# Kernel optimization log

Hardware: AMD Instinct MI355X
Metric: run time of the kernel (lower is better)

Reference implementation:

```python
import jax, jax.numpy as jnp
import numpy as np

B, T, E, V = 128, 24, 512, 30000
H2 = 2 * 512  # LSTMCell hidden size = 2*hidden_size per original code
IN = 2 * E    # token embedding concat image feature


def setup_inputs() -> dict:
    key = jax.random.key(0)
    ks = jax.random.split(key, 9)
    s = lambda fan: 1.0 / np.sqrt(fan)
    return {
        "features": jax.random.normal(ks[0], (B, E), jnp.float32),
        "captions": jax.random.randint(ks[1], (B, T), 0, V),
        "pad_idx": 0,
        "emb": jax.random.normal(ks[2], (V, E), jnp.float32),
        "W_ih": jax.random.uniform(ks[3], (4 * H2, IN), jnp.float32, -s(H2), s(H2)),
        "W_hh": jax.random.uniform(ks[4], (4 * H2, H2), jnp.float32, -s(H2), s(H2)),
        "b_ih": jax.random.uniform(ks[5], (4 * H2,), jnp.float32, -s(H2), s(H2)),
        "b_hh": jax.random.uniform(ks[6], (4 * H2,), jnp.float32, -s(H2), s(H2)),
        "W_out": jax.random.uniform(ks[7], (V, H2), jnp.float32, -s(H2), s(H2)),
        "b_out": jax.random.uniform(ks[8], (V,), jnp.float32, -s(H2), s(H2)),
    }


def reference(features, captions, pad_idx, emb, W_ih, W_hh, b_ih, b_hh, W_out, b_out):
    b = captions.shape[0]
    tok = emb[captions]                                   # [B,T,E]
    pad = jnp.broadcast_to(emb[pad_idx][None, None, :], (b, 1, E))
    seq = jnp.concatenate([pad, tok], axis=1)             # [B,T+1,E]
    feat = jnp.broadcast_to(features[:, None, :], (b, seq.shape[1], features.shape[1]))
    x = jnp.concatenate([seq, feat], axis=2)              # [B,T+1,2E]

    # precompute input-side gate projections for all timesteps (batched GEMM)
    xg = jnp.einsum('bti,gi->btg', x, W_ih) + b_ih + b_hh  # [B,T+1,4*H2]

    def step(carry, xg_t):
        h, c = carry
        g = xg_t + h @ W_hh.T                             # [B,4*H2]
        i, f, gg, o = jnp.split(g, 4, axis=-1)            # torch gate order i,f,g,o
        i, f, o = jax.nn.sigmoid(i), jax.nn.sigmoid(f), jax.nn.sigmoid(o)
        c = f * c + i * jnp.tanh(gg)
        h = o * jnp.tanh(c)
        return (h, c), h

    h0 = jnp.zeros((b, H2), x.dtype)
    c0 = jnp.zeros((b, H2), x.dtype)
    _, hs = jax.lax.scan(step, (h0, c0), jnp.swapaxes(xg, 0, 1))  # [T+1,B,H2]
    hs = jnp.swapaxes(hs, 0, 1)                           # [B,T+1,H2]

    logits = jnp.einsum('bth,vh->btv', hs, W_out) + b_out  # [B,T+1,V]
    predicted = jnp.transpose(logits[:, :-1, :], (0, 2, 1))  # [B,V,T]
    return predicted
```

## Files before the change

### kernel.cpp

```cpp
#include <hip/hip_runtime.h>
#include <hip/hip_bf16.h>
#include <math.h>

typedef unsigned short ushort_t;
typedef unsigned long long u64;
typedef __bf16 bf16x8 __attribute__((ext_vector_type(8)));
typedef float f32x4 __attribute__((ext_vector_type(4)));

#define BB 128
#define TT 24
#define EE 512
#define VV 30000
#define HH 1024
#define GG 4096
#define MM (BB*TT)
#define MPAD 30208

static __device__ __forceinline__ ushort_t f2bf(float x) {
  __hip_bfloat16 h = __float2bfloat16(x);
  return __builtin_bit_cast(ushort_t, h);
}

static __device__ __forceinline__ void gld_lds16(const void* g, void* l) {
  __builtin_amdgcn_global_load_lds((const __attribute__((address_space(1))) void*)g,
                                   (__attribute__((address_space(3))) void*)l, 16, 0, 0);
}


__global__ void cast_bf16_k(const float* __restrict__ s, ushort_t* __restrict__ d, int n4) {
  int i = blockIdx.x * blockDim.x + threadIdx.x;
  int stride = gridDim.x * blockDim.x;
  for (; i < n4; i += stride) {
    float4 v = reinterpret_cast<const float4*>(s)[i];
    ushort4 o;
    o.x = f2bf(v.x); o.y = f2bf(v.y); o.z = f2bf(v.z); o.w = f2bf(v.w);
    reinterpret_cast<ushort4*>(d)[i] = o;
  }
}

__global__ void bias_sum_k(const float* __restrict__ bi, const float* __restrict__ bh,
                           float* __restrict__ bs) {
  int i = blockIdx.x * blockDim.x + threadIdx.x;
  if (i < GG) bs[i] = bi[i] + bh[i];
}

__global__ void build_xa_k(const float* __restrict__ emb, const int* __restrict__ captions,
                           const int* __restrict__ pad_idx, const float* __restrict__ features,
                           ushort_t* __restrict__ xa) {
  int row = blockIdx.x;
  int t = row >> 7;
  int b = row & 127;
  int cap = (t == 0) ? pad_idx[0] : captions[b * TT + (t - 1)];
  const float* s0 = emb + (size_t)cap * EE;
  const float* s1 = features + (size_t)b * EE;
  ushort_t* d = xa + (size_t)row * (2 * EE);
  for (int e = threadIdx.x; e < EE; e += 256) {
    d[e] = f2bf(s0[e]);
    d[EE + e] = f2bf(s1[e]);
  }
}

__global__ void zero_bar_k(int* __restrict__ bar) {
  for (int i = threadIdx.x; i < 768; i += 256)
    __hip_atomic_store(&bar[i], 0, __ATOMIC_RELAXED, __HIP_MEMORY_SCOPE_AGENT);
}

__global__ __launch_bounds__(256) void gemm_xg(
    const ushort_t* __restrict__ A,
    const ushort_t* __restrict__ Bm,
    const float* __restrict__ bias,
    float* __restrict__ out,
    int M, int N, int swn, int xn_cnt)
{
  constexpr int K = 1024;
  __shared__ __align__(16) ushort_t As[2][8192];
  __shared__ __align__(16) ushort_t Bs[2][8192];
  const int bid = blockIdx.x;
  const int xcd = bid & 7, c = bid >> 3;
  const int xn = xcd % xn_cnt, xm = xcd / xn_cnt;
  const int nblk = xn * swn + (c % swn);
  const int n0 = nblk * 128;
  const int m0 = (xm * ((gridDim.x >> 3) / swn) + (c / swn)) * 128;
  const int tid = threadIdx.x, wid = tid >> 6, lane = tid & 63;
  const int wm = (wid >> 1) * 64, wn_ = (wid & 1) * 64;
  const int srow = lane >> 3;
  const int scolsw = ((lane & 7) ^ srow) * 8;
  const int rr = lane & 15, l4 = lane >> 4;
  const int swz = (rr & 7) << 4;
  const int col0 = (((l4 << 4) ^ swz) >> 1);
  const int col1 = (((64 | (l4 << 4)) ^ swz) >> 1);

  f32x4 acc[4][4] = {};

  auto stage = [&](int buf, int k0) {
    #pragma unroll
    for (int p = 0; p < 4; ++p) {
      int ch = p * 4 + wid;
      int row = ch * 8 + srow;
      gld_lds16(A + (size_t)(m0 + row) * K + k0 + scolsw, &As[buf][ch * 512]);
      gld_lds16(Bm + (size_t)(n0 + row) * K + k0 + scolsw, &Bs[buf][ch * 512]);
    }
  };

  stage(0, 0);
  int cur = 0;
  for (int tau = 0; tau < 16; ++tau) {
    if (tau < 15) {
      stage(cur ^ 1, (tau + 1) * 64);
      asm volatile("s_waitcnt vmcnt(8)" ::: "memory");
    } else {
      asm volatile("s_waitcnt vmcnt(0)" ::: "memory");
    }
    __builtin_amdgcn_s_barrier();
    const ushort_t* Ac = As[cur];
    const ushort_t* Bc = Bs[cur];
    #pragma unroll
    for (int kk = 0; kk < 2; ++kk) {
      const int ce = kk ? col1 : col0;
      bf16x8 af[4], bfv[4];
      #pragma unroll
      for (int i = 0; i < 4; ++i)
        af[i] = *reinterpret_cast<const bf16x8*>(Ac + (wm + i * 16 + rr) * 64 + ce);
      #pragma unroll
      for (int j = 0; j < 4; ++j)
        bfv[j] = *reinterpret_cast<const bf16x8*>(Bc + (wn_ + j * 16 + rr) * 64 + ce);
      #pragma unroll
      for (int i = 0; i < 4; ++i)
        #pragma unroll
        for (int j = 0; j < 4; ++j)
          acc[i][j] = __builtin_amdgcn_mfma_f32_16x16x32_bf16(af[i], bfv[j], acc[i][j], 0, 0, 0);
    }
    asm volatile("" ::: "memory");
    __builtin_amdgcn_s_barrier();
    cur ^= 1;
  }

  const int l16 = lane & 15;
  const int t_blk = m0 >> 7;
  #pragma unroll
  for (int i = 0; i < 4; ++i) {
    #pragma unroll
    for (int j = 0; j < 4; ++j) {
      int n = n0 + wn_ + j * 16 + l16;
      float bv = bias[n];
      #pragma unroll
      for (int r = 0; r < 4; ++r) {
        int b = wm + i * 16 + l4 * 4 + r;
        out[((size_t)t_blk * GG + n) * BB + b] = acc[i][j][r] + bv;
      }
    }
  }
}

__global__ __launch_bounds__(512) void gemm256_logits(
    const ushort_t* __restrict__ A,
    const ushort_t* __restrict__ Bm,
    const float* __restrict__ bias,
    float* __restrict__ out)
{
  constexpr int K = 1024, NT = 16;
  __shared__ __align__(16) ushort_t As[2][16384];
  __shared__ __align__(16) ushort_t Bs[2][16384];
  const int bid = blockIdx.x;
  const int g = (bid & 7) * 177 + (bid >> 3);
  const int m0 = (g / 12) * 256, n0 = (g % 12) * 256;
  const int tid = threadIdx.x, wid = tid >> 6, lane = tid & 63;
  const int wm2 = wid >> 2, wn4 = wid & 3;
  const int rr = lane & 15, l4 = lane >> 4;

  f32x4 acc[8][4] = {};

  auto stage = [&](int buf, int kt, int ct) {
    const int k0 = kt * 64;
    #pragma unroll
    for (int l = 0; l < 2; ++l) {
      int f = l * 512 + tid;
      int lr = f >> 3;
      int ecol = k0 + (((f & 7) ^ (lr & 7)) * 8);
      if (ct == 0 || ct == 3) {
        int cc = (ct == 3);
        int grow = (lr & 63) + ((lr >> 6) << 7) + cc * 64;
        gld_lds16(A + (size_t)(m0 + grow) * K + ecol,
                  &As[buf][cc * 8192 + (l * 512 + wid * 64) * 8]);
      } else {
        int cc = ct - 1;
        int grow = ((lr >> 5) << 6) + cc * 32 + (lr & 31);
        gld_lds16(Bm + (size_t)(n0 + grow) * K + ecol,
                  &Bs[buf][cc * 8192 + (l * 512 + wid * 64) * 8]);
      }
    }
  };
  auto rdA = [&](int buf, int mf, int kk) -> bf16x8 {
    int rl = wm2 * 64 + (mf & 3) * 16 + rr;
    return *reinterpret_cast<const bf16x8*>(
        &As[buf][(mf >> 2) * 8192 + rl * 64 + (((kk * 4 + l4) ^ (rr & 7)) * 8)]);
  };
  auto rdB = [&](int buf, int nf, int kk) -> bf16x8 {
    int rl = wn4 * 32 + (nf & 1) * 16 + rr;
    return *reinterpret_cast<const bf16x8*>(
        &Bs[buf][(nf >> 1) * 8192 + rl * 64 + (((kk * 4 + l4) ^ (rr & 7)) * 8)]);
  };

  #pragma unroll
  for (int hh = 0; hh < 4; ++hh) stage(0, 0, hh);
  asm volatile("s_waitcnt vmcnt(4)" ::: "memory");
  __builtin_amdgcn_s_barrier();

  bf16x8 aF[4][2], bF[2][2], bF2[2][2];
  int cur = 0;
  for (int g2 = 0; g2 < NT; ++g2) {
    const int buf = cur, bufn = cur ^ 1;
    const int ktn = (g2 + 1 < NT) ? g2 + 1 : g2;
    #pragma unroll
    for (int mf = 0; mf < 4; ++mf) { aF[mf][0] = rdA(buf, mf, 0); aF[mf][1] = rdA(buf, mf, 1); }
    #pragma unroll
    for (int nf = 0; nf < 2; ++nf) { bF[nf][0] = rdB(buf, nf, 0); bF[nf][1] = rdB(buf, nf, 1); }
    stage(bufn, ktn, 0);
    __builtin_amdgcn_s_barrier();
    asm volatile("s_waitcnt lgkmcnt(0)" ::: "memory");
    __builtin_amdgcn_sched_barrier(0);
    __builtin_amdgcn_s_setprio(1);
    #pragma unroll
    for (int mf = 0; mf < 4; ++mf)
      #pragma unroll
      for (int nf = 0; nf < 2; ++nf) {
        acc[mf][nf] = __builtin_amdgcn_mfma_f32_16x16x32_bf16(aF[mf][0], bF[nf][0], acc[mf][nf], 0, 0, 0);
        acc[mf][nf] = __builtin_amdgcn_mfma_f32_16x16x32_bf16(aF[mf][1], bF[nf][1], acc[mf][nf], 0, 0, 0);
      }
    __builtin_amdgcn_s_setprio(0);
    asm volatile("s_waitcnt vmcnt(4)" ::: "memory");
    __builtin_amdgcn_s_barrier();
    #pragma unroll
    for (int nf = 0; nf < 2; ++nf) { bF2[nf][0] = rdB(buf, 2 + nf, 0); bF2[nf][1] = rdB(buf, 2 + nf, 1); }
    stage(bufn, ktn, 1);
    __builtin_amdgcn_s_barrier();
    asm volatile("s_waitcnt lgkmcnt(0)" ::: "memory");
    __builtin_amdgcn_sched_barrier(0);
    __builtin_amdgcn_s_setprio(1);
    #pragma unroll
    for (int mf = 0; mf < 4; ++mf)
      #pragma unroll
      for (int nf = 0; nf < 2; ++nf) {
        acc[mf][2 + nf] = __builtin_amdgcn_mfma_f32_16x16x32_bf16(aF[mf][0], bF2[nf][0], acc[mf][2 + nf], 0, 0, 0);
        acc[mf][2 + nf] = __builtin_amdgcn_mfma_f32_16x16x32_bf16(aF[mf][1], bF2[nf][1], acc[mf][2 + nf], 0, 0, 0);
      }
    __builtin_amdgcn_s_setprio(0);
    asm volatile("s_waitcnt vmcnt(4)" ::: "memory");
    __builtin_amdgcn_s_barrier();
    #pragma unroll
    for (int mf = 0; mf < 4; ++mf) { aF[mf][0] = rdA(buf, 4 + mf, 0); aF[mf][1] = rdA(buf, 4 + mf, 1); }
    stage(bufn, ktn, 2);
    __builtin_amdgcn_s_barrier();
    asm volatile("s_waitcnt lgkmcnt(0)" ::: "memory");
    __builtin_amdgcn_sched_barrier(0);
    __builtin_amdgcn_s_setprio(1);
    #pragma unroll
    for (int mf = 0; mf < 4; ++mf)
      #pragma unroll
      for (int nf = 0; nf < 2; ++nf) {
        acc[4 + mf][nf] = __builtin_amdgcn_mfma_f32_16x16x32_bf16(aF[mf][0], bF[nf][0], acc[4 + mf][nf], 0, 0, 0);
        acc[4 + mf][nf] = __builtin_amdgcn_mfma_f32_16x16x32_bf16(aF[mf][1], bF[nf][1], acc[4 + mf][nf], 0, 0, 0);
      }
    __builtin_amdgcn_s_setprio(0);
    __builtin_amdgcn_s_barrier();
    stage(bufn, ktn, 3);
    __builtin_amdgcn_s_barrier();
    __builtin_amdgcn_s_setprio(1);
    #pragma unroll
    for (int mf = 0; mf < 4; ++mf)
      #pragma unroll
      for (int nf = 0; nf < 2; ++nf) {
        acc[4 + mf][2 + nf] = __builtin_amdgcn_mfma_f32_16x16x32_bf16(aF[mf][0], bF2[nf][0], acc[4 + mf][2 + nf], 0, 0, 0);
        acc[4 + mf][2 + nf] = __builtin_amdgcn_mfma_f32_16x16x32_bf16(aF[mf][1], bF2[nf][1], acc[4 + mf][2 + nf], 0, 0, 0);
      }
    __builtin_amdgcn_s_setprio(0);
    asm volatile("s_waitcnt vmcnt(4)" ::: "memory");
    __builtin_amdgcn_s_barrier();
    cur ^= 1;
  }
  asm volatile("s_waitcnt vmcnt(0)" ::: "memory");

  const int vbase = m0 + wm2 * 128;
  const int nbase = n0 + wn4 * 64;
  #pragma unroll
  for (int mf = 0; mf < 8; ++mf) {
    #pragma unroll
    for (int r = 0; r < 4; ++r) {
      int v = vbase + mf * 16 + l4 * 4 + r;
      if (v < VV) {
        float bv = bias[v];
        #pragma unroll
        for (int nf = 0; nf < 4; ++nf) {
          int n = nbase + nf * 16 + rr;
          int bb = n / TT, tq = n - bb * TT;
          out[(size_t)bb * ((size_t)VV * TT) + (size_t)v * TT + tq] = acc[mf][nf][r] + bv;
        }
      }
    }
  }
}

__global__ __launch_bounds__(512, 1) void lstm_seq_k(
    const ushort_t* __restrict__ Whh,
    const float* __restrict__ xgT,
    ushort_t* __restrict__ hs,
    int* __restrict__ bar)
{
  __shared__ f32x4 red[6][64][4];
  const int tid = threadIdx.x, wid = tid >> 6, lane = tid & 63;
  const int l16 = lane & 15, l4 = lane >> 4;
  const int bid = blockIdx.x;
  const int jblk = bid & 63, mblk = bid >> 6;
  const int j0 = jblk * 16, m0 = mblk * 32;
  const int ks = wid >> 1;
  const int msub = (wid & 1) * 16;
  int* flags = bar;
  int* rel = bar + 256;

  bf16x8 Breg[4][8];
  #pragma unroll
  for (int g = 0; g < 4; ++g) {
    const ushort_t* bp = Whh + ((size_t)(g * 1024 + j0 + l16) << 10) + ks * 256 + l4 * 8;
    #pragma unroll
    for (int kc = 0; kc < 8; ++kc)
      Breg[g][kc] = *reinterpret_cast<const bf16x8*>(bp + kc * 32);
  }
  const int arow = m0 + msub + l16;
  float c_reg[4] = {0.f, 0.f, 0.f, 0.f};

  for (int t = 0; t < TT; ++t) {
    f32x4 acc[4] = {};
    f32x4 xv[4];
    if (ks == 0) {
      const float* xp = xgT + ((size_t)(t * GG + j0 + l16)) * BB + m0 + msub + l4 * 4;
      #pragma unroll
      for (int g = 0; g < 4; ++g)
        xv[g] = *reinterpret_cast<const f32x4*>(xp + (size_t)g * 1024 * BB);
    }
    if (t > 0) {
      const u64* Ab = reinterpret_cast<const u64*>(
          hs + (((size_t)arow * TT + (t - 1)) << 10) + ks * 256 + l4 * 8);
      bf16x8 afs[8];
      #pragma unroll
      for (int kc = 0; kc < 8; ++kc) {
        union { u64 q[2]; bf16x8 v; } u;
        u.q[0] = __hip_atomic_load(Ab + kc * 8,     __ATOMIC_RELAXED, __HIP_MEMORY_SCOPE_AGENT);
        u.q[1] = __hip_atomic_load(Ab + kc * 8 + 1, __ATOMIC_RELAXED, __HIP_MEMORY_SCOPE_AGENT);
        afs[kc] = u.v;
      }
      #pragma unroll
      for (int kc = 0; kc < 8; ++kc)
        #pragma unroll
        for (int g = 0; g < 4; ++g)
          acc[g] = __builtin_amdgcn_mfma_f32_16x16x32_bf16(afs[kc], Breg[g][kc], acc[g], 0, 0, 0);
    }
    if (ks != 0) {
      int slot = (ks - 1) * 2 + (wid & 1);
      #pragma unroll
      for (int g = 0; g < 4; ++g) red[slot][lane][g] = acc[g];
    }
    __syncthreads();
    if (ks == 0) {
      #pragma unroll
      for (int s = 0; s < 3; ++s)
        #pragma unroll
        for (int g = 0; g < 4; ++g)
          acc[g] += red[s * 2 + (wid & 1)][lane][g];
      #pragma unroll
      for (int r = 0; r < 4; ++r) {
        int b = m0 + msub + l4 * 4 + r;
        float gi = acc[0][r] + xv[0][r];
        float gf = acc[1][r] + xv[1][r];
        float gg = acc[2][r] + xv[2][r];
        float go = acc[3][r] + xv[3][r];
        gi = 1.f / (1.f + expf(-gi));
        gf = 1.f / (1.f + expf(-gf));
        go = 1.f / (1.f + expf(-go));
        float cn = gf * c_reg[r] + gi * tanhf(gg);
        c_reg[r] = cn;
        float hn = go * tanhf(cn);
        unsigned hv = (unsigned)f2bf(hn);
        unsigned pv = (unsigned)__shfl_xor((int)hv, 1);
        if (!(l16 & 1)) {
          unsigned pk = (hv & 0xffffu) | (pv << 16);
          __hip_atomic_store(
              reinterpret_cast<unsigned*>(hs + (((size_t)b * TT + t) << 10) + j0 + l16),
              pk, __ATOMIC_RELAXED, __HIP_MEMORY_SCOPE_AGENT);
        }
      }
    }
    if (t < TT - 1) {
      __syncthreads();
      if (bid == 0) {
        if (wid == 0) {
          if (lane == 0)
            __hip_atomic_store(&flags[0], t + 1, __ATOMIC_RELAXED, __HIP_MEMORY_SCOPE_AGENT);
          for (;;) {
            int a0 = __hip_atomic_load(&flags[lane],       __ATOMIC_RELAXED, __HIP_MEMORY_SCOPE_AGENT);
            int a1 = __hip_atomic_load(&flags[lane +  64], __ATOMIC_RELAXED, __HIP_MEMORY_SCOPE_AGENT);
            int a2 = __hip_atomic_load(&flags[lane + 128], __ATOMIC_RELAXED, __HIP_MEMORY_SCOPE_AGENT);
            int a3 = __hip_atomic_load(&flags[lane + 192], __ATOMIC_RELAXED, __HIP_MEMORY_SCOPE_AGENT);
            int mn = min(min(a0, a1), min(a2, a3));
            if (__all(mn >= t + 1)) break;
            __builtin_amdgcn_s_sleep(2);
          }
          if (lane < 8)
            __hip_atomic_store(&rel[lane * 64], t + 1, __ATOMIC_RELAXED, __HIP_MEMORY_SCOPE_AGENT);
        }
      } else {
        if (tid == 0) {
          __hip_atomic_store(&flags[bid], t + 1, __ATOMIC_RELAXED, __HIP_MEMORY_SCOPE_AGENT);
          while (__hip_atomic_load(&rel[(bid & 7) * 64], __ATOMIC_RELAXED, __HIP_MEMORY_SCOPE_AGENT) < t + 1)
            __builtin_amdgcn_s_sleep(4);
        }
      }
      __syncthreads();
    }
  }
}


extern "C" void kernel_launch(void* const* d_in, const int* in_sizes, int n_in,
                              void* d_out, int out_size, void* d_ws, size_t ws_size,
                              hipStream_t stream) {
  const float* features = (const float*)d_in[0];
  const int*   captions = (const int*)d_in[1];
  const int*   pad_idx  = (const int*)d_in[2];
  const float* emb      = (const float*)d_in[3];
  const float* W_ih     = (const float*)d_in[4];
  const float* W_hh     = (const float*)d_in[5];
  const float* b_ih     = (const float*)d_in[6];
  const float* b_hh     = (const float*)d_in[7];
  const float* W_out    = (const float*)d_in[8];
  const float* b_out    = (const float*)d_in[9];
  float* out = (float*)d_out;

  char* w = (char*)d_ws;
  auto carve = [&](size_t bytes) {
    char* p = w;
    w += (bytes + 255) & ~(size_t)255;
    return p;
  };
  ushort_t* Wih_b  = (ushort_t*)carve((size_t)GG * HH * 2);
  ushort_t* Whh_b  = (ushort_t*)carve((size_t)GG * HH * 2);
  ushort_t* Wout_b = (ushort_t*)carve((size_t)MPAD * HH * 2);
  ushort_t* xa     = (ushort_t*)carve((size_t)MM * HH * 2);
  float*    xgT    = (float*)carve((size_t)MM * GG * 4);
  ushort_t* hs     = (ushort_t*)carve((size_t)MM * HH * 2);
  float*    bsum   = (float*)carve((size_t)GG * 4);
  int*      bar    = (int*)carve(4096);

  cast_bf16_k<<<dim3(1024), 256, 0, stream>>>(W_ih, Wih_b, GG * HH / 4);
  cast_bf16_k<<<dim3(1024), 256, 0, stream>>>(W_hh, Whh_b, GG * HH / 4);
  cast_bf16_k<<<dim3(2048), 256, 0, stream>>>(W_out, Wout_b, VV * HH / 4);
  bias_sum_k<<<dim3(16), 256, 0, stream>>>(b_ih, b_hh, bsum);
  build_xa_k<<<dim3(MM), 256, 0, stream>>>(emb, captions, pad_idx, features, xa);
  zero_bar_k<<<dim3(1), 256, 0, stream>>>(bar);

  gemm_xg<<<dim3(768), 256, 0, stream>>>(xa, Wih_b, bsum, xgT, MM, GG, 8, 4);

  lstm_seq_k<<<dim3(256), 512, 0, stream>>>(Whh_b, xgT, hs, bar);

  gemm256_logits<<<dim3(1416), 512, 0, stream>>>(Wout_b, hs, b_out, out);
}
```

Before: 563.3 us.

## Fuse prep casts, swap xg GEMM operands, use flat barrier in LSTM

Merges the three weight-cast kernels and the bias-sum kernel into one launch. It swaps the operands of the input-gate GEMM so the gate dimension indexes rows, with a new block-to-tile mapping and a matching output layout. The LSTM's centralized barrier (block 0 gathers and releases) is replaced by a flat barrier where each block polls only the 64 flags for its own m-block, which is meant to cut per-step sync latency. The logits epilogue hoists the division used in output index computation out of the store loop.

```diff
diff --git a/kernel.cpp b/kernel.cpp
--- a/kernel.cpp
+++ b/kernel.cpp
@@ -26,22 +26,29 @@
                                    (__attribute__((address_space(3))) void*)l, 16, 0, 0);
 }
 
-
-__global__ void cast_bf16_k(const float* __restrict__ s, ushort_t* __restrict__ d, int n4) {
-  int i = blockIdx.x * blockDim.x + threadIdx.x;
-  int stride = gridDim.x * blockDim.x;
-  for (; i < n4; i += stride) {
+__global__ void prep_k(const float* __restrict__ Wih, const float* __restrict__ Whh,
+                       const float* __restrict__ Wout,
+                       const float* __restrict__ bi, const float* __restrict__ bh,
+                       ushort_t* __restrict__ Wih_b, ushort_t* __restrict__ Whh_b,
+                       ushort_t* __restrict__ Wout_b, float* __restrict__ bs) {
+  const int bid = blockIdx.x, tid = threadIdx.x;
+  const float* s; ushort_t* d; int n4, i0, stride;
+  if (bid < 2048) {
+    s = Wout; d = Wout_b; n4 = VV * HH / 4; i0 = bid * 256 + tid; stride = 2048 * 256;
+  } else if (bid < 2560) {
+    s = Wih; d = Wih_b; n4 = GG * HH / 4; i0 = (bid - 2048) * 256 + tid; stride = 512 * 256;
+  } else if (bid < 3072) {
+    s = Whh; d = Whh_b; n4 = GG * HH / 4; i0 = (bid - 2560) * 256 + tid; stride = 512 * 256;
+  } else {
+    for (int i = tid; i < GG; i += 256) bs[i] = bi[i] + bh[i];
+    return;
+  }
+  for (int i = i0; i < n4; i += stride) {
     float4 v = reinterpret_cast<const float4*>(s)[i];
     ushort4 o;
     o.x = f2bf(v.x); o.y = f2bf(v.y); o.z = f2bf(v.z); o.w = f2bf(v.w);
     reinterpret_cast<ushort4*>(d)[i] = o;
   }
-}
-
-__global__ void bias_sum_k(const float* __restrict__ bi, const float* __restrict__ bh,
-                           float* __restrict__ bs) {
-  int i = blockIdx.x * blockDim.x + threadIdx.x;
-  if (i < GG) bs[i] = bi[i] + bh[i];
 }
 
 __global__ void build_xa_k(const float* __restrict__ emb, const int* __restrict__ captions,
@@ -61,7 +68,7 @@
 }
 
 __global__ void zero_bar_k(int* __restrict__ bar) {
-  for (int i = threadIdx.x; i < 768; i += 256)
+  for (int i = threadIdx.x; i < 1024; i += 256)
     __hip_atomic_store(&bar[i], 0, __ATOMIC_RELAXED, __HIP_MEMORY_SCOPE_AGENT);
 }
 
@@ -69,18 +76,15 @@
     const ushort_t* __restrict__ A,
     const ushort_t* __restrict__ Bm,
     const float* __restrict__ bias,
-    float* __restrict__ out,
-    int M, int N, int swn, int xn_cnt)
+    float* __restrict__ out)
 {
   constexpr int K = 1024;
   __shared__ __align__(16) ushort_t As[2][8192];
   __shared__ __align__(16) ushort_t Bs[2][8192];
   const int bid = blockIdx.x;
-  const int xcd = bid & 7, c = bid >> 3;
-  const int xn = xcd % xn_cnt, xm = xcd / xn_cnt;
-  const int nblk = xn * swn + (c % swn);
-  const int n0 = nblk * 128;
-  const int m0 = (xm * ((gridDim.x >> 3) / swn) + (c / swn)) * 128;
+  const int g = (bid & 7) * 96 + (bid >> 3);
+  const int m0 = (g / 24) * 128;
+  const int n0 = (g % 24) * 128;
   const int tid = threadIdx.x, wid = tid >> 6, lane = tid & 63;
   const int wm = (wid >> 1) * 64, wn_ = (wid & 1) * 64;
   const int srow = lane >> 3;
@@ -136,17 +140,16 @@
   }
 
   const int l16 = lane & 15;
-  const int t_blk = m0 >> 7;
   #pragma unroll
   for (int i = 0; i < 4; ++i) {
     #pragma unroll
-    for (int j = 0; j < 4; ++j) {
-      int n = n0 + wn_ + j * 16 + l16;
-      float bv = bias[n];
-      #pragma unroll
-      for (int r = 0; r < 4; ++r) {
-        int b = wm + i * 16 + l4 * 4 + r;
-        out[((size_t)t_blk * GG + n) * BB + b] = acc[i][j][r] + bv;
+    for (int r = 0; r < 4; ++r) {
+      int gi = m0 + wm + i * 16 + l4 * 4 + r;
+      float bv = bias[gi];
+      #pragma unroll
+      for (int j = 0; j < 4; ++j) {
+        int col = n0 + wn_ + j * 16 + l16;
+        out[((size_t)(col >> 7) * GG + gi) * BB + (col & 127)] = acc[i][j][r] + bv;
       }
     }
   }
@@ -282,6 +285,13 @@
 
   const int vbase = m0 + wm2 * 128;
   const int nbase = n0 + wn4 * 64;
+  size_t obase[4];
+  #pragma unroll
+  for (int nf = 0; nf < 4; ++nf) {
+    int n = nbase + nf * 16 + rr;
+    int bb = n / TT, tq = n - bb * TT;
+    obase[nf] = (size_t)bb * ((size_t)VV * TT) + tq;
+  }
   #pragma unroll
   for (int mf = 0; mf < 8; ++mf) {
     #pragma unroll
@@ -290,11 +300,8 @@
       if (v < VV) {
         float bv = bias[v];
         #pragma unroll
-        for (int nf = 0; nf < 4; ++nf) {
-          int n = nbase + nf * 16 + rr;
-          int bb = n / TT, tq = n - bb * TT;
-          out[(size_t)bb * ((size_t)VV * TT) + (size_t)v * TT + tq] = acc[mf][nf][r] + bv;
-        }
+        for (int nf = 0; nf < 4; ++nf)
+          out[obase[nf] + (size_t)v * TT] = acc[mf][nf][r] + bv;
       }
     }
   }
@@ -315,7 +322,7 @@
   const int ks = wid >> 1;
   const int msub = (wid & 1) * 16;
   int* flags = bar;
-  int* rel = bar + 256;
+  const int fidx = (mblk << 6) | (ks << 4) | l16;
 
   bf16x8 Breg[4][8];
   #pragma unroll
@@ -391,30 +398,13 @@
     }
     if (t < TT - 1) {
       __syncthreads();
-      if (bid == 0) {
-        if (wid == 0) {
-          if (lane == 0)
-            __hip_atomic_store(&flags[0], t + 1, __ATOMIC_RELAXED, __HIP_MEMORY_SCOPE_AGENT);
-          for (;;) {
-            int a0 = __hip_atomic_load(&flags[lane],       __ATOMIC_RELAXED, __HIP_MEMORY_SCOPE_AGENT);
-            int a1 = __hip_atomic_load(&flags[lane +  64], __ATOMIC_RELAXED, __HIP_MEMORY_SCOPE_AGENT);
-            int a2 = __hip_atomic_load(&flags[lane + 128], __ATOMIC_RELAXED, __HIP_MEMORY_SCOPE_AGENT);
-            int a3 = __hip_atomic_load(&flags[lane + 192], __ATOMIC_RELAXED, __HIP_MEMORY_SCOPE_AGENT);
-            int mn = min(min(a0, a1), min(a2, a3));
-            if (__all(mn >= t + 1)) break;
-            __builtin_amdgcn_s_sleep(2);
-          }
-          if (lane < 8)
-            __hip_atomic_store(&rel[lane * 64], t + 1, __ATOMIC_RELAXED, __HIP_MEMORY_SCOPE_AGENT);
-        }
-      } else {
-        if (tid == 0) {
-          __hip_atomic_store(&flags[bid], t + 1, __ATOMIC_RELAXED, __HIP_MEMORY_SCOPE_AGENT);
-          while (__hip_atomic_load(&rel[(bid & 7) * 64], __ATOMIC_RELAXED, __HIP_MEMORY_SCOPE_AGENT) < t + 1)
-            __builtin_amdgcn_s_sleep(4);
-        }
-      }
-      __syncthreads();
+      if (tid == 0)
+        __hip_atomic_store(&flags[bid], t + 1, __ATOMIC_RELAXED, __HIP_MEMORY_SCOPE_AGENT);
+      for (;;) {
+        int a = __hip_atomic_load(&flags[fidx], __ATOMIC_RELAXED, __HIP_MEMORY_SCOPE_AGENT);
+        if (__all(a >= t + 1)) break;
+        __builtin_amdgcn_s_sleep(1);
+      }
     }
   }
 }
@@ -448,16 +438,14 @@
   float*    xgT    = (float*)carve((size_t)MM * GG * 4);
   ushort_t* hs     = (ushort_t*)carve((size_t)MM * HH * 2);
   float*    bsum   = (float*)carve((size_t)GG * 4);
-  int*      bar    = (int*)carve(4096);
-
-  cast_bf16_k<<<dim3(1024), 256, 0, stream>>>(W_ih, Wih_b, GG * HH / 4);
-  cast_bf16_k<<<dim3(1024), 256, 0, stream>>>(W_hh, Whh_b, GG * HH / 4);
-  cast_bf16_k<<<dim3(2048), 256, 0, stream>>>(W_out, Wout_b, VV * HH / 4);
-  bias_sum_k<<<dim3(16), 256, 0, stream>>>(b_ih, b_hh, bsum);
+  int*      bar    = (int*)carve(16384);
+
+  prep_k<<<dim3(3073), 256, 0, stream>>>(W_ih, W_hh, W_out, b_ih, b_hh,
+                                         Wih_b, Whh_b, Wout_b, bsum);
   build_xa_k<<<dim3(MM), 256, 0, stream>>>(emb, captions, pad_idx, features, xa);
   zero_bar_k<<<dim3(1), 256, 0, stream>>>(bar);
 
-  gemm_xg<<<dim3(768), 256, 0, stream>>>(xa, Wih_b, bsum, xgT, MM, GG, 8, 4);
+  gemm_xg<<<dim3(768), 256, 0, stream>>>(Wih_b, xa, bsum, xgT);
 
   lstm_seq_k<<<dim3(256), 512, 0, stream>>>(Whh_b, xgT, hs, bar);
 
```

Measured after the change: 571.7 us. No clear change (+1.5%).
